# Kernel tuning notes

Measured on AMD Instinct MI355X. Metric: run time of the kernel, lower is better.

The kernel has to match this reference:

```python
import jax, jax.numpy as jnp
import numpy as np

N_MLP = 16
LATENT = 1024
S0, S1, S2, OUT = 512, 256, 128, 3


def _make_grid(n_grid_step):
    # matches np.meshgrid (indexing='xy') then reshape(-1): points (x, y)
    p = np.linspace(-1.0, 1.0, n_grid_step, dtype=np.float32)
    X, Y = np.meshgrid(p, p)
    return jnp.asarray(np.stack([X.ravel(), Y.ravel()], axis=-1))  # [G, 2]


def setup_inputs() -> dict:
    key = jax.random.key(0)
    ks = jax.random.split(key, 12)
    sc = lambda fan_in: 1.0 / np.sqrt(fan_in)
    inp = {
        "x0": jax.random.normal(ks[0], (LATENT,), jnp.float32),
        "W0a": jax.random.normal(ks[1], (N_MLP, S0, LATENT), jnp.float32) * sc(LATENT),
        "b0a": jax.random.normal(ks[2], (N_MLP, S0), jnp.float32) * sc(LATENT),
        "W0b": jax.random.normal(ks[3], (N_MLP, S0, 2), jnp.float32) * sc(2),
        "b0b": jax.random.normal(ks[4], (N_MLP, S0), jnp.float32) * sc(2),
        "W1": jax.random.normal(ks[5], (N_MLP, S1, S0), jnp.float32) * sc(S0),
        "b1": jax.random.normal(ks[6], (N_MLP, S1), jnp.float32) * sc(S0),
        "W2": jax.random.normal(ks[7], (N_MLP, S2, S1), jnp.float32) * sc(S1),
        "b2": jax.random.normal(ks[8], (N_MLP, S2), jnp.float32) * sc(S1),
        "W3": jax.random.normal(ks[9], (N_MLP, OUT, S2), jnp.float32) * sc(S2),
        "b3": jax.random.normal(ks[10], (N_MLP, OUT), jnp.float32) * sc(S2),
        "n_grid_step": 128,
    }
    return inp


def reference(x0, W0a, b0a, W0b, b0b, W1, b1, W2, b2, W3, b3, n_grid_step):
    grid = _make_grid(n_grid_step)  # [G, 2], constant (requires_grad=False)
    # latent branch: [m, S0]
    y0_a = jnp.einsum('mol,l->mo', W0a, x0) + b0a
    # grid branch: [m, G, S0]
    y0_b = jnp.einsum('moi,gi->mgo', W0b, grid) + b0b[:, None, :]
    h = jax.nn.relu(y0_a[:, None, :] + y0_b)                        # [m,G,S0]
    h = jax.nn.relu(jnp.einsum('moh,mgh->mgo', W1, h) + b1[:, None, :])  # [m,G,S1]
    h = jax.nn.relu(jnp.einsum('moh,mgh->mgo', W2, h) + b2[:, None, :])  # [m,G,S2]
    out = jnp.tanh(jnp.einsum('moh,mgh->mgo', W3, h) + b3[:, None, :])   # [m,G,3]
    return out.reshape(-1, OUT)  # [m*G, 3]
```

## Files before the change

### kernel.cpp

```cpp
#include <hip/hip_runtime.h>
#include <hip/hip_bf16.h>
#include <cstdint>

typedef __bf16 bf16_t;
typedef bf16_t bf16x8 __attribute__((ext_vector_type(8)));
typedef bf16_t bf16x4 __attribute__((ext_vector_type(4)));
typedef float  f32x4  __attribute__((ext_vector_type(4)));

#define S0 512
#define S1 256
#define S2 128
#define NGRID 128
#define GPTS (NGRID*NGRID)

#define WS_BASE 0u
#define WS_W1P  32768u
#define WS_W2P  (32768u + 4194304u)
#define WS_W3P  (32768u + 4194304u + 1048576u)

__device__ __forceinline__ float tanh_fast(float x) {
  float e = __builtin_amdgcn_exp2f(x * 2.88539008f);
  return fmaf(-2.0f, __builtin_amdgcn_rcpf(e + 1.0f), 1.0f);
}

__global__ __launch_bounds__(256) void prep_k(
    const float* __restrict__ x0, const float* __restrict__ W0a,
    const float* __restrict__ b0a, const float* __restrict__ b0b,
    const float* __restrict__ W1, const float* __restrict__ W2,
    const float* __restrict__ W3, float* __restrict__ base,
    bf16_t* __restrict__ W1p, bf16_t* __restrict__ W2p, bf16_t* __restrict__ W3p)
{
  if (blockIdx.x < 2048) {
    int wid = (blockIdx.x << 2) + (threadIdx.x >> 6);
    int L = threadIdx.x & 63;
    int m = wid >> 9, o = wid & 511;
    const float* wrow = W0a + ((size_t)(m*S0 + o) << 10);
    float acc = 0.f;
#pragma unroll
    for (int i = 0; i < 4; ++i) {
      f32x4 wv = *(const f32x4*)(wrow + i*256 + L*4);
      f32x4 xv = *(const f32x4*)(x0   + i*256 + L*4);
      acc += wv.x*xv.x + wv.y*xv.y + wv.z*xv.z + wv.w*xv.w;
    }
#pragma unroll
    for (int s = 32; s; s >>= 1) acc += __shfl_xor(acc, s, 64);
    if (L == 0) base[m*S0 + o] = acc + b0a[m*S0 + o] + b0b[m*S0 + o];
    return;
  }

  int T = (blockIdx.x - 2048) * 256 + threadIdx.x;
  const float* src = nullptr;
  bf16_t* dst = nullptr;
  if (T < 262144) {
    int L = T & 63, nt = (T >> 6) & 15, ks = (T >> 10) & 15, m = T >> 14;
    int n = nt*16 + (L & 15), k0 = ks*32 + ((L >> 4) & 3)*8;
    src = W1 + (size_t)(m*S1 + n)*S0 + k0;
    dst = W1p + (size_t)T*8;
  } else if (T < 262144 + 65536) {
    int T2 = T - 262144;
    int L = T2 & 63, nt = (T2 >> 6) & 7, ks = (T2 >> 9) & 7, m = T2 >> 12;
    int n = nt*16 + (L & 15), k0 = ks*32 + ((L >> 4) & 3)*8;
    src = W2 + (size_t)(m*S2 + n)*S1 + k0;
    dst = W2p + (size_t)T2*8;
  } else {
    int T3 = T - 327680;
    int L = T3 & 63, ks = (T3 >> 6) & 3, m = T3 >> 8;
    int n = L & 15, k0 = ks*32 + ((L >> 4) & 3)*8;
    dst = W3p + (size_t)T3*8;
    if (n < 3) src = W3 + (size_t)(m*3 + n)*S2 + k0;
  }
  bf16x8 v;
  if (src) {
    f32x4 a = *(const f32x4*)src;
    f32x4 b = *(const f32x4*)(src + 4);
    v[0]=(bf16_t)a.x; v[1]=(bf16_t)a.y; v[2]=(bf16_t)a.z; v[3]=(bf16_t)a.w;
    v[4]=(bf16_t)b.x; v[5]=(bf16_t)b.y; v[6]=(bf16_t)b.z; v[7]=(bf16_t)b.w;
  } else {
#pragma unroll
    for (int j = 0; j < 8; ++j) v[j] = (bf16_t)0.f;
  }
  *(bf16x8*)dst = v;
}

__global__ __launch_bounds__(256, 3) void fused_mlp_k(
    const float* __restrict__ base, const float* __restrict__ W0b,
    const bf16_t* __restrict__ W1p, const bf16_t* __restrict__ W2p,
    const bf16_t* __restrict__ W3p,
    const float* __restrict__ b1, const float* __restrict__ b2,
    const float* __restrict__ b3, float* __restrict__ out)
{
  __shared__ __align__(16) bf16_t sA1[64*264];

  const int bid  = blockIdx.x;
  const int m    = bid >> 8;
  const int tile = bid & 255;
  const int g0   = tile * 64;

  const int tid  = threadIdx.x;
  const int w    = tid >> 6, L = tid & 63;
  const int quad = L >> 4, lrow = L & 15;

  const float step = 2.0f / 127.0f;
  const float yv  = -1.0f + (float)(tile >> 1) * step;
  const float xv0 = -1.0f + (float)(((tile & 1) << 6) + lrow) * step;

  const float* basep = base + m*S0;
  const float* w0bp  = W0b + (size_t)m*S0*2;

  f32x4 zero = {0.f, 0.f, 0.f, 0.f};
  f32x4 acc1[4][4];
#pragma unroll
  for (int a = 0; a < 4; ++a)
#pragma unroll
    for (int b = 0; b < 4; ++b) acc1[a][b] = zero;

  const bf16_t* bp1 = W1p + (((size_t)(m*16)*16 + w*4)*64 + L)*8;
  bf16x8 Bc[4];
#pragma unroll
  for (int n = 0; n < 4; ++n) Bc[n] = *(const bf16x8*)(bp1 + (size_t)n*512);

#pragma unroll 2
  for (int ks = 0; ks < 16; ++ks) {
    const int kk = ks*32 + quad*8;
    f32x4 cA  = *(const f32x4*)(basep + kk);
    f32x4 cB  = *(const f32x4*)(basep + kk + 4);
    f32x4 wv0 = *(const f32x4*)(w0bp + kk*2);
    f32x4 wv1 = *(const f32x4*)(w0bp + kk*2 + 4);
    f32x4 wv2 = *(const f32x4*)(w0bp + kk*2 + 8);
    f32x4 wv3 = *(const f32x4*)(w0bp + kk*2 + 12);

    bf16x8 Bn[4];
    if (ks < 15) {
#pragma unroll
      for (int n = 0; n < 4; ++n)
        Bn[n] = *(const bf16x8*)(bp1 + (size_t)(ks+1)*8192 + (size_t)n*512);
    }

    float t[8], wx[8];
    t[0] = fmaf(wv0.y, yv, cA.x); wx[0] = wv0.x;
    t[1] = fmaf(wv0.w, yv, cA.y); wx[1] = wv0.z;
    t[2] = fmaf(wv1.y, yv, cA.z); wx[2] = wv1.x;
    t[3] = fmaf(wv1.w, yv, cA.w); wx[3] = wv1.z;
    t[4] = fmaf(wv2.y, yv, cB.x); wx[4] = wv2.x;
    t[5] = fmaf(wv2.w, yv, cB.y); wx[5] = wv2.z;
    t[6] = fmaf(wv3.y, yv, cB.z); wx[6] = wv3.x;
    t[7] = fmaf(wv3.w, yv, cB.w); wx[7] = wv3.z;

#pragma unroll
    for (int mt = 0; mt < 4; ++mt) {
      const float xr = xv0 + (float)(mt*16)*step;
      bf16x8 af;
#pragma unroll
      for (int j = 0; j < 8; ++j)
        af[j] = (bf16_t)fmaxf(fmaf(wx[j], xr, t[j]), 0.f);
#pragma unroll
      for (int n = 0; n < 4; ++n)
        acc1[mt][n] = __builtin_amdgcn_mfma_f32_16x16x32_bf16(Bc[n], af, acc1[mt][n], 0, 0, 0);
    }
    if (ks < 15) {
#pragma unroll
      for (int n = 0; n < 4; ++n) Bc[n] = Bn[n];
    }
  }

#pragma unroll
  for (int nb = 0; nb < 4; ++nb) {
    const int col = w*64 + nb*16 + quad*4;
    f32x4 bb = *(const f32x4*)(b1 + m*S1 + col);
#pragma unroll
    for (int mt = 0; mt < 4; ++mt) {
      const int row = mt*16 + lrow;
      bf16x4 v;
#pragma unroll
      for (int p = 0; p < 4; ++p)
        v[p] = (bf16_t)fmaxf(acc1[mt][nb][p] + bb[p], 0.f);
      *(bf16x4*)(&sA1[row*264 + col]) = v;
    }
  }
  __syncthreads();

  f32x4 acc2[4][2];
#pragma unroll
  for (int a = 0; a < 4; ++a) { acc2[a][0] = zero; acc2[a][1] = zero; }
  const bf16_t* bp2 = W2p + (((size_t)(m*8)*8 + w*2)*64 + L)*8;
#pragma unroll 2
  for (int ks = 0; ks < 8; ++ks) {
    const int k2 = ks*32 + quad*8;
    bf16x8 af[4];
#pragma unroll
    for (int mt = 0; mt < 4; ++mt)
      af[mt] = *(const bf16x8*)(&sA1[(mt*16 + lrow)*264 + k2]);
    bf16x8 b0f = *(const bf16x8*)(bp2 + (size_t)ks*4096);
    bf16x8 b1f = *(const bf16x8*)(bp2 + (size_t)ks*4096 + 512);
#pragma unroll
    for (int mt = 0; mt < 4; ++mt)
      acc2[mt][0] = __builtin_amdgcn_mfma_f32_16x16x32_bf16(b0f, af[mt], acc2[mt][0], 0, 0, 0);
#pragma unroll
    for (int mt = 0; mt < 4; ++mt)
      acc2[mt][1] = __builtin_amdgcn_mfma_f32_16x16x32_bf16(b1f, af[mt], acc2[mt][1], 0, 0, 0);
  }
  __syncthreads();

  bf16_t* sH2 = sA1;
#pragma unroll
  for (int nb = 0; nb < 2; ++nb) {
    const int col = w*32 + nb*16 + quad*4;
    f32x4 bb = *(const f32x4*)(b2 + m*S2 + col);
#pragma unroll
    for (int mt = 0; mt < 4; ++mt) {
      const int row = mt*16 + lrow;
      bf16x4 v;
#pragma unroll
      for (int p = 0; p < 4; ++p)
        v[p] = (bf16_t)fmaxf(acc2[mt][nb][p] + bb[p], 0.f);
      *(bf16x4*)(&sH2[row*136 + col]) = v;
    }
  }
  __syncthreads();

  f32x4 acc3 = zero;
#pragma unroll
  for (int ks = 0; ks < 4; ++ks) {
    bf16x8 af  = *(const bf16x8*)(&sH2[(w*16 + lrow)*136 + ks*32 + quad*8]);
    bf16x8 bfr = *(const bf16x8*)(W3p + (((size_t)m*4 + ks)*64 + L)*8);
    acc3 = __builtin_amdgcn_mfma_f32_16x16x32_bf16(bfr, af, acc3, 0, 0, 0);
  }
  if (quad == 0) {
    const size_t o = ((size_t)m*GPTS + g0 + w*16 + lrow)*3;
    out[o + 0] = tanh_fast(acc3[0] + b3[m*3 + 0]);
    out[o + 1] = tanh_fast(acc3[1] + b3[m*3 + 1]);
    out[o + 2] = tanh_fast(acc3[2] + b3[m*3 + 2]);
  }
}

extern "C" void kernel_launch(void* const* d_in, const int* in_sizes, int n_in,
                              void* d_out, int out_size, void* d_ws, size_t ws_size,
                              hipStream_t stream) {
  const float* x0  = (const float*)d_in[0];
  const float* W0a = (const float*)d_in[1];
  const float* b0a = (const float*)d_in[2];
  const float* W0b = (const float*)d_in[3];
  const float* b0b = (const float*)d_in[4];
  const float* W1  = (const float*)d_in[5];
  const float* b1  = (const float*)d_in[6];
  const float* W2  = (const float*)d_in[7];
  const float* b2  = (const float*)d_in[8];
  const float* W3  = (const float*)d_in[9];
  const float* b3  = (const float*)d_in[10];

  char* ws = (char*)d_ws;
  float*  base = (float*)(ws + WS_BASE);
  bf16_t* W1p  = (bf16_t*)(ws + WS_W1P);
  bf16_t* W2p  = (bf16_t*)(ws + WS_W2P);
  bf16_t* W3p  = (bf16_t*)(ws + WS_W3P);
  float*  out  = (float*)d_out;

  prep_k<<<3344, 256, 0, stream>>>(x0, W0a, b0a, b0b, W1, W2, W3, base, W1p, W2p, W3p);
  fused_mlp_k<<<4096, 256, 0, stream>>>(base, W0b, W1p, W2p, W3p, b1, b2, b3, out);
}
```

Baseline: 206.8 us.

## Swizzle LDS, deinterleave W0b, coalesce weight packing, raise occupancy

Several changes land together. The padded shared-memory rows are replaced by XOR-swizzled layouts to avoid bank conflicts with less LDS. W0b is split into separate x/y arrays in the workspace when space allows, so loads are contiguous. The W1/W2 packing in the prep kernel now uses coalesced row-wise reads, and packed bf16 conversion is used throughout. The kernel's occupancy hint goes from 3 to 4 blocks per CU, and the explicit B-fragment double buffering in layer 1 is removed, which may expose load latency.

```diff
diff --git a/kernel.cpp b/kernel.cpp
--- a/kernel.cpp
+++ b/kernel.cpp
@@ -4,35 +4,60 @@
 
 typedef __bf16 bf16_t;
 typedef bf16_t bf16x8 __attribute__((ext_vector_type(8)));
-typedef bf16_t bf16x4 __attribute__((ext_vector_type(4)));
 typedef float  f32x4  __attribute__((ext_vector_type(4)));
+typedef float  f32x2  __attribute__((ext_vector_type(2)));
+typedef unsigned int u32;
+typedef u32 u32x4 __attribute__((ext_vector_type(4)));
+typedef u32 u32x2 __attribute__((ext_vector_type(2)));
 
 #define S0 512
 #define S1 256
 #define S2 128
-#define NGRID 128
-#define GPTS (NGRID*NGRID)
+#define GPTS 16384
 
 #define WS_BASE 0u
 #define WS_W1P  32768u
 #define WS_W2P  (32768u + 4194304u)
 #define WS_W3P  (32768u + 4194304u + 1048576u)
-
+#define WS_OLD_END (32768u + 4194304u + 1048576u + 65536u)
+#define WS_W0BX WS_OLD_END
+#define WS_W0BY (WS_OLD_END + 32768u)
+#define WS_NEED (WS_OLD_END + 65536u)
+
+__device__ __forceinline__ u32 pkcvt(float lo, float hi) {
+  __hip_bfloat162 h = __float22bfloat162_rn(make_float2(lo, hi));
+  u32 u;
+  __builtin_memcpy(&u, &h, 4);
+  return u;
+}
 __device__ __forceinline__ float tanh_fast(float x) {
   float e = __builtin_amdgcn_exp2f(x * 2.88539008f);
   return fmaf(-2.0f, __builtin_amdgcn_rcpf(e + 1.0f), 1.0f);
 }
+__device__ __forceinline__ int swzA(int row, int col) {
+  int ch = col >> 3;
+  ch = (ch & ~7) | ((ch ^ row) & 7);
+  return (row << 8) + (ch << 3) + (col & 7);
+}
+__device__ __forceinline__ int swzH(int row, int col) {
+  int ch = col >> 3;
+  ch = (ch & ~7) | ((ch ^ row) & 7);
+  return (row << 7) + (ch << 3) + (col & 7);
+}
 
 __global__ __launch_bounds__(256) void prep_k(
     const float* __restrict__ x0, const float* __restrict__ W0a,
     const float* __restrict__ b0a, const float* __restrict__ b0b,
+    const float* __restrict__ W0b,
     const float* __restrict__ W1, const float* __restrict__ W2,
     const float* __restrict__ W3, float* __restrict__ base,
-    bf16_t* __restrict__ W1p, bf16_t* __restrict__ W2p, bf16_t* __restrict__ W3p)
+    bf16_t* __restrict__ W1p, bf16_t* __restrict__ W2p, bf16_t* __restrict__ W3p,
+    float* __restrict__ W0bx, float* __restrict__ W0by, int deint)
 {
-  if (blockIdx.x < 2048) {
-    int wid = (blockIdx.x << 2) + (threadIdx.x >> 6);
-    int L = threadIdx.x & 63;
+  const int bid = blockIdx.x, tid = threadIdx.x;
+  const int w = tid >> 6, L = tid & 63;
+  if (bid < 2048) {
+    int wid = (bid << 2) + w;
     int m = wid >> 9, o = wid & 511;
     const float* wrow = W0a + ((size_t)(m*S0 + o) << 10);
     float acc = 0.f;
@@ -45,51 +70,60 @@
 #pragma unroll
     for (int s = 32; s; s >>= 1) acc += __shfl_xor(acc, s, 64);
     if (L == 0) base[m*S0 + o] = acc + b0a[m*S0 + o] + b0b[m*S0 + o];
-    return;
-  }
-
-  int T = (blockIdx.x - 2048) * 256 + threadIdx.x;
-  const float* src = nullptr;
-  bf16_t* dst = nullptr;
-  if (T < 262144) {
-    int L = T & 63, nt = (T >> 6) & 15, ks = (T >> 10) & 15, m = T >> 14;
-    int n = nt*16 + (L & 15), k0 = ks*32 + ((L >> 4) & 3)*8;
-    src = W1 + (size_t)(m*S1 + n)*S0 + k0;
-    dst = W1p + (size_t)T*8;
-  } else if (T < 262144 + 65536) {
-    int T2 = T - 262144;
-    int L = T2 & 63, nt = (T2 >> 6) & 7, ks = (T2 >> 9) & 7, m = T2 >> 12;
-    int n = nt*16 + (L & 15), k0 = ks*32 + ((L >> 4) & 3)*8;
-    src = W2 + (size_t)(m*S2 + n)*S1 + k0;
-    dst = W2p + (size_t)T2*8;
-  } else {
-    int T3 = T - 327680;
-    int L = T3 & 63, ks = (T3 >> 6) & 3, m = T3 >> 8;
-    int n = L & 15, k0 = ks*32 + ((L >> 4) & 3)*8;
-    dst = W3p + (size_t)T3*8;
-    if (n < 3) src = W3 + (size_t)(m*3 + n)*S2 + k0;
-  }
-  bf16x8 v;
-  if (src) {
+  } else if (bid < 2064) {
+    if (!deint) return;
+    int T = (bid - 2048)*256 + tid;
+    int m = T >> 8, p = (T & 255) << 1;
+    f32x4 v = *(const f32x4*)(W0b + ((size_t)m*S0 + p)*2);
+    *(f32x2*)(W0bx + m*S0 + p) = (f32x2){v.x, v.z};
+    *(f32x2*)(W0by + m*S0 + p) = (f32x2){v.y, v.w};
+  } else if (bid < 3088) {
+    int wid = (bid - 2064)*4 + w;
+    int m = wid >> 8, n = wid & 255;
+    const float* src = W1 + ((size_t)(m*S1 + n) << 9) + L*8;
     f32x4 a = *(const f32x4*)src;
     f32x4 b = *(const f32x4*)(src + 4);
-    v[0]=(bf16_t)a.x; v[1]=(bf16_t)a.y; v[2]=(bf16_t)a.z; v[3]=(bf16_t)a.w;
-    v[4]=(bf16_t)b.x; v[5]=(bf16_t)b.y; v[6]=(bf16_t)b.z; v[7]=(bf16_t)b.w;
+    u32x4 pu;
+    pu[0] = pkcvt(a.x, a.y); pu[1] = pkcvt(a.z, a.w);
+    pu[2] = pkcvt(b.x, b.y); pu[3] = pkcvt(b.z, b.w);
+    int ks = L >> 2, quad = L & 3, nt = n >> 4, lrow = n & 15;
+    *(u32x4*)(W1p + (((size_t)(m*16 + ks)*16 + nt)*64 + quad*16 + lrow)*8) = pu;
+  } else if (bid < 3600) {
+    int wid = (bid - 3088)*4 + w;
+    int m = wid >> 7, n = wid & 127;
+    const float* src = W2 + ((size_t)(m*S2 + n) << 8) + L*4;
+    f32x4 a = *(const f32x4*)src;
+    u32x2 pu; pu[0] = pkcvt(a.x, a.y); pu[1] = pkcvt(a.z, a.w);
+    int ks = L >> 3, quad = (L >> 1) & 3, half = L & 1, nt = n >> 4, lrow = n & 15;
+    *(u32x2*)(W2p + (((size_t)(m*8 + ks)*8 + nt)*64 + quad*16 + lrow)*8 + half*4) = pu;
   } else {
-#pragma unroll
-    for (int j = 0; j < 8; ++j) v[j] = (bf16_t)0.f;
-  }
-  *(bf16x8*)dst = v;
-}
-
-__global__ __launch_bounds__(256, 3) void fused_mlp_k(
+    int T3 = (bid - 3600)*256 + tid;
+    int l = T3 & 63, ks = (T3 >> 6) & 3, m = T3 >> 8;
+    int n = l & 15, k0 = ks*32 + ((l >> 4) & 3)*8;
+    bf16x8 v;
+    if (n < 3) {
+      const float* src = W3 + (size_t)(m*3 + n)*S2 + k0;
+      f32x4 a = *(const f32x4*)src;
+      f32x4 b = *(const f32x4*)(src + 4);
+      v[0]=(bf16_t)a.x; v[1]=(bf16_t)a.y; v[2]=(bf16_t)a.z; v[3]=(bf16_t)a.w;
+      v[4]=(bf16_t)b.x; v[5]=(bf16_t)b.y; v[6]=(bf16_t)b.z; v[7]=(bf16_t)b.w;
+    } else {
+#pragma unroll
+      for (int j = 0; j < 8; ++j) v[j] = (bf16_t)0.f;
+    }
+    *(bf16x8*)(W3p + (size_t)T3*8) = v;
+  }
+}
+
+__global__ __launch_bounds__(256, 4) void fused_mlp_k(
     const float* __restrict__ base, const float* __restrict__ W0b,
+    const float* __restrict__ wxa, const float* __restrict__ wya, int deint,
     const bf16_t* __restrict__ W1p, const bf16_t* __restrict__ W2p,
     const bf16_t* __restrict__ W3p,
     const float* __restrict__ b1, const float* __restrict__ b2,
     const float* __restrict__ b3, float* __restrict__ out)
 {
-  __shared__ __align__(16) bf16_t sA1[64*264];
+  __shared__ __align__(16) bf16_t sA1[64*256];
 
   const int bid  = blockIdx.x;
   const int m    = bid >> 8;
@@ -106,60 +140,58 @@
 
   const float* basep = base + m*S0;
   const float* w0bp  = W0b + (size_t)m*S0*2;
-
-  f32x4 zero = {0.f, 0.f, 0.f, 0.f};
+  const float* wxp   = wxa + m*S0;
+  const float* wyp   = wya + m*S0;
+
+  const f32x4 zero4 = {0.f, 0.f, 0.f, 0.f};
   f32x4 acc1[4][4];
 #pragma unroll
   for (int a = 0; a < 4; ++a)
 #pragma unroll
-    for (int b = 0; b < 4; ++b) acc1[a][b] = zero;
+    for (int b = 0; b < 4; ++b) acc1[a][b] = zero4;
 
   const bf16_t* bp1 = W1p + (((size_t)(m*16)*16 + w*4)*64 + L)*8;
-  bf16x8 Bc[4];
-#pragma unroll
-  for (int n = 0; n < 4; ++n) Bc[n] = *(const bf16x8*)(bp1 + (size_t)n*512);
+  const f32x4 yv4 = {yv, yv, yv, yv};
 
 #pragma unroll 2
   for (int ks = 0; ks < 16; ++ks) {
     const int kk = ks*32 + quad*8;
-    f32x4 cA  = *(const f32x4*)(basep + kk);
-    f32x4 cB  = *(const f32x4*)(basep + kk + 4);
-    f32x4 wv0 = *(const f32x4*)(w0bp + kk*2);
-    f32x4 wv1 = *(const f32x4*)(w0bp + kk*2 + 4);
-    f32x4 wv2 = *(const f32x4*)(w0bp + kk*2 + 8);
-    f32x4 wv3 = *(const f32x4*)(w0bp + kk*2 + 12);
-
-    bf16x8 Bn[4];
-    if (ks < 15) {
-#pragma unroll
-      for (int n = 0; n < 4; ++n)
-        Bn[n] = *(const bf16x8*)(bp1 + (size_t)(ks+1)*8192 + (size_t)n*512);
-    }
-
-    float t[8], wx[8];
-    t[0] = fmaf(wv0.y, yv, cA.x); wx[0] = wv0.x;
-    t[1] = fmaf(wv0.w, yv, cA.y); wx[1] = wv0.z;
-    t[2] = fmaf(wv1.y, yv, cA.z); wx[2] = wv1.x;
-    t[3] = fmaf(wv1.w, yv, cA.w); wx[3] = wv1.z;
-    t[4] = fmaf(wv2.y, yv, cB.x); wx[4] = wv2.x;
-    t[5] = fmaf(wv2.w, yv, cB.y); wx[5] = wv2.z;
-    t[6] = fmaf(wv3.y, yv, cB.z); wx[6] = wv3.x;
-    t[7] = fmaf(wv3.w, yv, cB.w); wx[7] = wv3.z;
+    bf16x8 Bf[4];
+    const bf16_t* bp = bp1 + (size_t)ks*8192;
+#pragma unroll
+    for (int n = 0; n < 4; ++n) Bf[n] = *(const bf16x8*)(bp + n*512);
+
+    f32x4 c0 = *(const f32x4*)(basep + kk);
+    f32x4 c1 = *(const f32x4*)(basep + kk + 4);
+    f32x4 wx0v, wx1v, wy0v, wy1v;
+    if (deint) {
+      wx0v = *(const f32x4*)(wxp + kk); wx1v = *(const f32x4*)(wxp + kk + 4);
+      wy0v = *(const f32x4*)(wyp + kk); wy1v = *(const f32x4*)(wyp + kk + 4);
+    } else {
+      f32x4 a = *(const f32x4*)(w0bp + kk*2);
+      f32x4 b = *(const f32x4*)(w0bp + kk*2 + 4);
+      f32x4 c = *(const f32x4*)(w0bp + kk*2 + 8);
+      f32x4 d = *(const f32x4*)(w0bp + kk*2 + 12);
+      wx0v = (f32x4){a.x, a.z, b.x, b.z}; wy0v = (f32x4){a.y, a.w, b.y, b.w};
+      wx1v = (f32x4){c.x, c.z, d.x, d.z}; wy1v = (f32x4){c.y, c.w, d.y, d.w};
+    }
+    f32x4 t0 = __builtin_elementwise_fma(wy0v, yv4, c0);
+    f32x4 t1 = __builtin_elementwise_fma(wy1v, yv4, c1);
 
 #pragma unroll
     for (int mt = 0; mt < 4; ++mt) {
       const float xr = xv0 + (float)(mt*16)*step;
+      const f32x4 xr4 = {xr, xr, xr, xr};
+      f32x4 h0 = __builtin_elementwise_max(__builtin_elementwise_fma(wx0v, xr4, t0), zero4);
+      f32x4 h1 = __builtin_elementwise_max(__builtin_elementwise_fma(wx1v, xr4, t1), zero4);
+      u32x4 au;
+      au[0] = pkcvt(h0.x, h0.y); au[1] = pkcvt(h0.z, h0.w);
+      au[2] = pkcvt(h1.x, h1.y); au[3] = pkcvt(h1.z, h1.w);
       bf16x8 af;
-#pragma unroll
-      for (int j = 0; j < 8; ++j)
-        af[j] = (bf16_t)fmaxf(fmaf(wx[j], xr, t[j]), 0.f);
+      __builtin_memcpy(&af, &au, 16);
 #pragma unroll
       for (int n = 0; n < 4; ++n)
-        acc1[mt][n] = __builtin_amdgcn_mfma_f32_16x16x32_bf16(Bc[n], af, acc1[mt][n], 0, 0, 0);
-    }
-    if (ks < 15) {
-#pragma unroll
-      for (int n = 0; n < 4; ++n) Bc[n] = Bn[n];
+        acc1[mt][n] = __builtin_amdgcn_mfma_f32_16x16x32_bf16(Bf[n], af, acc1[mt][n], 0, 0, 0);
     }
   }
 
@@ -170,18 +202,16 @@
 #pragma unroll
     for (int mt = 0; mt < 4; ++mt) {
       const int row = mt*16 + lrow;
-      bf16x4 v;
-#pragma unroll
-      for (int p = 0; p < 4; ++p)
-        v[p] = (bf16_t)fmaxf(acc1[mt][nb][p] + bb[p], 0.f);
-      *(bf16x4*)(&sA1[row*264 + col]) = v;
+      f32x4 v = __builtin_elementwise_max(acc1[mt][nb] + bb, zero4);
+      u32x2 s; s[0] = pkcvt(v.x, v.y); s[1] = pkcvt(v.z, v.w);
+      *(u32x2*)(&sA1[swzA(row, col)]) = s;
     }
   }
   __syncthreads();
 
   f32x4 acc2[4][2];
 #pragma unroll
-  for (int a = 0; a < 4; ++a) { acc2[a][0] = zero; acc2[a][1] = zero; }
+  for (int a = 0; a < 4; ++a) { acc2[a][0] = zero4; acc2[a][1] = zero4; }
   const bf16_t* bp2 = W2p + (((size_t)(m*8)*8 + w*2)*64 + L)*8;
 #pragma unroll 2
   for (int ks = 0; ks < 8; ++ks) {
@@ -189,7 +219,7 @@
     bf16x8 af[4];
 #pragma unroll
     for (int mt = 0; mt < 4; ++mt)
-      af[mt] = *(const bf16x8*)(&sA1[(mt*16 + lrow)*264 + k2]);
+      af[mt] = *(const bf16x8*)(&sA1[swzA(mt*16 + lrow, k2)]);
     bf16x8 b0f = *(const bf16x8*)(bp2 + (size_t)ks*4096);
     bf16x8 b1f = *(const bf16x8*)(bp2 + (size_t)ks*4096 + 512);
 #pragma unroll
@@ -209,19 +239,17 @@
 #pragma unroll
     for (int mt = 0; mt < 4; ++mt) {
       const int row = mt*16 + lrow;
-      bf16x4 v;
-#pragma unroll
-      for (int p = 0; p < 4; ++p)
-        v[p] = (bf16_t)fmaxf(acc2[mt][nb][p] + bb[p], 0.f);
-      *(bf16x4*)(&sH2[row*136 + col]) = v;
+      f32x4 v = __builtin_elementwise_max(acc2[mt][nb] + bb, zero4);
+      u32x2 s; s[0] = pkcvt(v.x, v.y); s[1] = pkcvt(v.z, v.w);
+      *(u32x2*)(&sH2[swzH(row, col)]) = s;
     }
   }
   __syncthreads();
 
-  f32x4 acc3 = zero;
+  f32x4 acc3 = zero4;
 #pragma unroll
   for (int ks = 0; ks < 4; ++ks) {
-    bf16x8 af  = *(const bf16x8*)(&sH2[(w*16 + lrow)*136 + ks*32 + quad*8]);
+    bf16x8 af  = *(const bf16x8*)(&sH2[swzH(w*16 + lrow, ks*32 + quad*8)]);
     bf16x8 bfr = *(const bf16x8*)(W3p + (((size_t)m*4 + ks)*64 + L)*8);
     acc3 = __builtin_amdgcn_mfma_f32_16x16x32_bf16(bfr, af, acc3, 0, 0, 0);
   }
@@ -253,8 +281,13 @@
   bf16_t* W1p  = (bf16_t*)(ws + WS_W1P);
   bf16_t* W2p  = (bf16_t*)(ws + WS_W2P);
   bf16_t* W3p  = (bf16_t*)(ws + WS_W3P);
+  float*  W0bx = (float*)(ws + WS_W0BX);
+  float*  W0by = (float*)(ws + WS_W0BY);
   float*  out  = (float*)d_out;
-
-  prep_k<<<3344, 256, 0, stream>>>(x0, W0a, b0a, b0b, W1, W2, W3, base, W1p, W2p, W3p);
-  fused_mlp_k<<<4096, 256, 0, stream>>>(base, W0b, W1p, W2p, W3p, b1, b2, b3, out);
-}
+  int deint = (ws_size >= (size_t)WS_NEED) ? 1 : 0;
+
+  prep_k<<<3616, 256, 0, stream>>>(x0, W0a, b0a, b0b, W0b, W1, W2, W3,
+                                   base, W1p, W2p, W3p, W0bx, W0by, deint);
+  fused_mlp_k<<<4096, 256, 0, stream>>>(base, W0b, W0bx, W0by, deint,
+                                        W1p, W2p, W3p, b1, b2, b3, out);
+}
```

Result: slower. 331.9 us (+60.5%).
